# Kernel optimization log

Hardware: AMD Instinct MI355X
Metric: run time of the kernel (lower is better)

Reference implementation:

```python
import jax, jax.numpy as jnp
import numpy as np

C = 256
CQK = C // 8


def setup_inputs() -> dict:
    key = jax.random.key(0)
    ks = jax.random.split(key, 8)
    B, H, W = 4, 64, 64
    x = jax.random.normal(ks[0], (B, C, H, W), dtype=jnp.float32)
    # 1x1 conv weights are plain [out_c, in_c] matrices + bias
    sq = 1.0 / np.sqrt(C)
    Wq = jax.random.uniform(ks[1], (CQK, C), jnp.float32, -sq, sq)
    bq = jax.random.uniform(ks[2], (CQK,), jnp.float32, -sq, sq)
    Wk = jax.random.uniform(ks[3], (CQK, C), jnp.float32, -sq, sq)
    bk = jax.random.uniform(ks[4], (CQK,), jnp.float32, -sq, sq)
    Wv = jax.random.uniform(ks[5], (C, C), jnp.float32, -sq, sq)
    bv = jax.random.uniform(ks[6], (C,), jnp.float32, -sq, sq)
    gamma = jnp.zeros((1,), dtype=jnp.float32)
    return {"x": x, "Wq": Wq, "bq": bq, "Wk": Wk, "bk": bk, "Wv": Wv, "bv": bv, "gamma": gamma}


def reference(x, Wq, bq, Wk, bk, Wv, bv, gamma):
    B, Cc, H, W = x.shape
    N = H * W
    xf = x.reshape(B, Cc, N)  # [B, C, N]
    # 1x1 convs == channel GEMMs
    q = jnp.einsum('dc,bcn->bdn', Wq, xf) + bq[None, :, None]  # [B, C/8, N]
    k = jnp.einsum('dc,bcn->bdn', Wk, xf) + bk[None, :, None]  # [B, C/8, N]
    v = jnp.einsum('dc,bcn->bdn', Wv, xf) + bv[None, :, None]  # [B, C, N]
    # attention[b, i, j] = softmax_j( q_i . k_j )  (no scaling, as in source)
    attn = jax.nn.softmax(jnp.einsum('bdn,bdm->bnm', q, k), axis=-1)  # [B, N, N]
    # out = value @ attention  (note: NOT attention^T, faithful to source)
    out = jnp.einsum('bcn,bnm->bcm', v, attn)  # [B, C, N]
    out = out.reshape(B, Cc, H, W)
    return gamma[0] * out + x
```

## Files before the change

kernel.cpp:

```cpp
#include <hip/hip_runtime.h>
#include <hip/hip_bf16.h>


#define NB 4
#define CC 256
#define NN 4096
#define L2E 1.44269504088896340f

typedef short  short4v  __attribute__((ext_vector_type(4)));
typedef short  short8v  __attribute__((ext_vector_type(8)));
typedef __bf16 bf16x8   __attribute__((ext_vector_type(8)));
typedef float  f32x4    __attribute__((ext_vector_type(4)));
typedef float  f32x16   __attribute__((ext_vector_type(16)));
typedef unsigned long u64x2 __attribute__((ext_vector_type(2)));
typedef unsigned int u32;

static __device__ __forceinline__ unsigned short f2bf(float f) {
  union { __bf16 h; unsigned short u; } v; v.h = (__bf16)f; return v.u;
}
static __device__ __forceinline__ float bf2f(unsigned short u) {
  union { unsigned u; float f; } v; v.u = (u32)u << 16; return v.f;
}

union FragU { short8v s; bf16x8 b; unsigned u[4]; };

static __device__ __forceinline__ bf16x8 ld_frag(const unsigned short* p) {
  FragU u; u.s = *(const short8v*)p; return u.b;
}

static __device__ __forceinline__ f32x16 zero16() {
  f32x16 v;
#pragma unroll
  for (int i = 0; i < 16; ++i) v[i] = 0.0f;
  return v;
}

static __device__ __forceinline__ f32x16 mfma32(bf16x8 a, bf16x8 b, f32x16 c) {
  return __builtin_amdgcn_mfma_f32_32x32x16_bf16(a, b, c, 0, 0, 0);
}
static __device__ __forceinline__ f32x16 mfma8(long a, long b, f32x16 c) {
  return __builtin_amdgcn_mfma_f32_32x32x16_fp8_fp8(a, b, c, 0, 0, 0);
}

__global__ __launch_bounds__(256) void k_wcvt(
    const float* __restrict__ Wq, const float* __restrict__ Wk,
    const float* __restrict__ Wv, unsigned short* __restrict__ Wb)
{
  const int i4 = blockIdx.x * 256 + threadIdx.x;
  const int e = i4 * 4;
  const int row = e >> 8, c = e & 255;
  const float* src = (row < 32) ? (Wq + row * 256 + c)
                   : (row < 64) ? (Wk + (row - 32) * 256 + c)
                                : (Wv + (row - 64) * 256 + c);
  f32x4 v = *(const f32x4*)src;
  short4v s;
#pragma unroll
  for (int j = 0; j < 4; ++j) s[j] = (short)f2bf(v[j]);
  *(short4v*)(Wb + e) = s;
}

__global__ __launch_bounds__(256) void k_proj(
    const float* __restrict__ x, const unsigned short* __restrict__ Wb,
    const float* __restrict__ bq, const float* __restrict__ bk,
    const float* __restrict__ bv,
    unsigned short* __restrict__ Qt, unsigned short* __restrict__ Kt,
    unsigned char* __restrict__ V8)
{
  __shared__ unsigned short xs[32][268];
  const int t = threadIdx.x;
  const int b = blockIdx.y;
  const int n0 = blockIdx.x * 32;
  const int w = t >> 6, l = t & 63, h = l >> 5, col = l & 31;

  const float* xb = x + (size_t)b * CC * NN;
  {
    const int c_off = t >> 3, nl = 4 * (t & 7);
#pragma unroll
    for (int c0 = 0; c0 < CC; c0 += 32) {
      int c = c0 + c_off;
      f32x4 v4 = *(const f32x4*)(xb + (size_t)c * NN + n0 + nl);
#pragma unroll
      for (int j = 0; j < 4; ++j) xs[nl + j][c] = f2bf(v4[j]);
    }
  }
  __syncthreads();

  for (int f = w; f < 10; f += 4) {
    const float* bsrc; int rowbase; int mode; int wrow;
    if (f == 0)      { bsrc = bq; rowbase = 0;            mode = 0; wrow = 0; }
    else if (f == 1) { bsrc = bk; rowbase = 0;            mode = 1; wrow = 32; }
    else             { bsrc = bv; rowbase = (f - 2) * 32; mode = 2; wrow = 64 + rowbase; }

    f32x16 acc0 = zero16();
    const unsigned short* wr = Wb + (size_t)(wrow + col) * 256 + 8 * h;

#pragma unroll
    for (int k0 = 0; k0 < CC; k0 += 16) {
      FragU a;
      a.s = *(const short8v*)(wr + k0);
      const unsigned short* p0 = &xs[col][k0 + 8 * h];
      FragU b0;
      short4v t0a = *(const short4v*)p0, t0b = *(const short4v*)(p0 + 4);
#pragma unroll
      for (int j = 0; j < 4; ++j) { b0.s[j] = t0a[j]; b0.s[4 + j] = t0b[j]; }
      acc0 = mfma32(a.b, b0.b, acc0);
    }

    const int n = n0 + col;
#pragma unroll
    for (int q = 0; q < 4; ++q) {
      f32x4 bias4 = *(const f32x4*)(bsrc + rowbase + 8 * q + 4 * h);
      float vals[4];
#pragma unroll
      for (int i = 0; i < 4; ++i) vals[i] = acc0[4 * q + i] + bias4[i];
      if (mode == 2) {
        const size_t tb = ((((size_t)b * 128 + (n >> 5)) * 2 + ((n >> 3) & 1)) * 256) * 16
                          + ((n >> 4) & 1) * 8 + (n & 7);
        u32 w01 = __builtin_amdgcn_cvt_pk_fp8_f32(vals[0], vals[1], 0, false);
        u32 w23 = __builtin_amdgcn_cvt_pk_fp8_f32(vals[2], vals[3], 0, false);
        const int cb0 = rowbase + 8 * q + 4 * h;
        V8[tb + (size_t)(cb0 + 0) * 16] = (unsigned char)(w01 & 0xff);
        V8[tb + (size_t)(cb0 + 1) * 16] = (unsigned char)((w01 >> 8) & 0xff);
        V8[tb + (size_t)(cb0 + 2) * 16] = (unsigned char)(w23 & 0xff);
        V8[tb + (size_t)(cb0 + 3) * 16] = (unsigned char)((w23 >> 8) & 0xff);
      } else {
        unsigned short* dst = (mode == 0) ? Qt : Kt;
        const float scale = (mode == 0) ? L2E : 1.0f;
        short4v s4;
#pragma unroll
        for (int i = 0; i < 4; ++i) s4[i] = (short)f2bf(vals[i] * scale);
        *(short4v*)(dst + ((size_t)b * NN + n) * 32 + 8 * q + 4 * h) = s4;
      }
    }
  }
}

__global__ __launch_bounds__(512) void k_rowstats(
    const unsigned short* __restrict__ Qt, const unsigned short* __restrict__ Kt,
    float* __restrict__ cbias)
{
  __shared__ float ssum[8][64];
  const int t = threadIdx.x;
  const int w = t >> 6, l = t & 63, h = l >> 5, col = l & 31;
  const int b = blockIdx.y;
  const int n0 = blockIdx.x * 64;
  const unsigned short* Qb = Qt + (size_t)b * NN * 32;
  const unsigned short* Kb = Kt + (size_t)b * NN * 32;

  bf16x8 bq00 = ld_frag(Qb + (size_t)(n0 + col) * 32 + 8 * h);
  bf16x8 bq01 = ld_frag(Qb + (size_t)(n0 + col) * 32 + 16 + 8 * h);
  bf16x8 bq10 = ld_frag(Qb + (size_t)(n0 + 32 + col) * 32 + 8 * h);
  bf16x8 bq11 = ld_frag(Qb + (size_t)(n0 + 32 + col) * 32 + 16 + 8 * h);

  float acc0 = 0.0f, acc1 = 0.0f;
  const int mbase = w * (NN / 8);
#pragma unroll 2
  for (int mt = 0; mt < 16; ++mt) {
    const int m0 = mbase + mt * 32;
    bf16x8 ak0 = ld_frag(Kb + (size_t)(m0 + col) * 32 + 8 * h);
    bf16x8 ak1 = ld_frag(Kb + (size_t)(m0 + col) * 32 + 16 + 8 * h);
    f32x16 S0 = zero16(), S1 = zero16();
    S0 = mfma32(ak0, bq00, S0);
    S0 = mfma32(ak1, bq01, S0);
    S1 = mfma32(ak0, bq10, S1);
    S1 = mfma32(ak1, bq11, S1);
    float p0 = 0.0f, p1 = 0.0f, p2 = 0.0f, p3 = 0.0f;
#pragma unroll
    for (int r = 0; r < 8; ++r) {
      p0 += __builtin_amdgcn_exp2f(S0[r]);
      p1 += __builtin_amdgcn_exp2f(S0[8 + r]);
      p2 += __builtin_amdgcn_exp2f(S1[r]);
      p3 += __builtin_amdgcn_exp2f(S1[8 + r]);
    }
    acc0 += p0 + p1;
    acc1 += p2 + p3;
  }
  acc0 += __shfl_xor(acc0, 32);
  acc1 += __shfl_xor(acc1, 32);

  if (l < 32) { ssum[w][l] = acc0; ssum[w][32 + l] = acc1; }
  __syncthreads();

  if (t < 64) {
    float s = 0.0f;
#pragma unroll
    for (int wv = 0; wv < 8; ++wv) s += ssum[wv][t];
    cbias[(size_t)b * NN + n0 + t] = -__builtin_amdgcn_logf(s);
  }
}

__global__ __launch_bounds__(512) void k_emat(
    const unsigned short* __restrict__ Qt, const unsigned short* __restrict__ Kt,
    const float* __restrict__ cbias, unsigned char* __restrict__ E8)
{
  const int t = threadIdx.x;
  const int w = t >> 6, l = t & 63, h = l >> 5, col = l & 31;
  const int b = blockIdx.y;
  const int n0 = blockIdx.x * 32;
  const unsigned short* Qb = Qt + (size_t)b * NN * 32;
  const unsigned short* Kb = Kt + (size_t)b * NN * 32;

  bf16x8 aq0 = ld_frag(Qb + (size_t)(n0 + col) * 32 + 8 * h);
  bf16x8 aq1 = ld_frag(Qb + (size_t)(n0 + col) * 32 + 16 + 8 * h);

  f32x4 cb4[4];
  const float* cbi = cbias + (size_t)b * NN + n0;
#pragma unroll
  for (int q = 0; q < 4; ++q) cb4[q] = *(const f32x4*)(cbi + 8 * q + 4 * h);

  unsigned char* st = E8 + ((size_t)b * 512 + 2 * (size_t)(n0 >> 4) + h) * 32768;

#pragma unroll 2
  for (int mt = 0; mt < 16; ++mt) {
    const int m0 = w * 512 + mt * 32;
    bf16x8 bk0 = ld_frag(Kb + (size_t)(m0 + col) * 32 + 8 * h);
    bf16x8 bk1 = ld_frag(Kb + (size_t)(m0 + col) * 32 + 16 + 8 * h);
    f32x16 S = zero16();
    S = mfma32(aq0, bk0, S);
    S = mfma32(aq1, bk1, S);

    float e[16];
#pragma unroll
    for (int q = 0; q < 4; ++q)
#pragma unroll
      for (int i = 0; i < 4; ++i)
        e[4 * q + i] = __builtin_amdgcn_exp2f(S[4 * q + i] + cb4[q][i]);

    u32 wA = __builtin_amdgcn_cvt_pk_fp8_f32(e[0], e[1], 0, false);
    wA = __builtin_amdgcn_cvt_pk_fp8_f32(e[2], e[3], wA, true);
    u32 wB = __builtin_amdgcn_cvt_pk_fp8_f32(e[4], e[5], 0, false);
    wB = __builtin_amdgcn_cvt_pk_fp8_f32(e[6], e[7], wB, true);
    u32 wC = __builtin_amdgcn_cvt_pk_fp8_f32(e[8], e[9], 0, false);
    wC = __builtin_amdgcn_cvt_pk_fp8_f32(e[10], e[11], wC, true);
    u32 wD = __builtin_amdgcn_cvt_pk_fp8_f32(e[12], e[13], 0, false);
    wD = __builtin_amdgcn_cvt_pk_fp8_f32(e[14], e[15], wD, true);
    asm("v_permlane32_swap_b32 %0, %1" : "+v"(wA), "+v"(wB));
    asm("v_permlane32_swap_b32 %0, %1" : "+v"(wC), "+v"(wD));
    unsigned long ev0 = ((unsigned long)wB << 32) | wA;
    unsigned long ev1 = ((unsigned long)wD << 32) | wC;

    *(unsigned long*)(st + (size_t)(m0 + col) * 8) = ev0;
    *(unsigned long*)(st + 65536 + (size_t)(m0 + col) * 8) = ev1;
  }
}

__global__ __launch_bounds__(512) void k_pv(
    const unsigned char* __restrict__ E8, const unsigned char* __restrict__ V8,
    const float* __restrict__ x, const float* __restrict__ gamma,
    float* __restrict__ out)
{
  __shared__ unsigned short ldb[64][264];
  const int t = threadIdx.x;
  const int w = t >> 6, l = t & 63, h = l >> 5, col = l & 31;
  const int b = blockIdx.y;
  const int m0 = blockIdx.x * 64;
  const int mf = w & 1, cc = (w >> 1) * 64;

  const unsigned char* ep = E8 + ((size_t)b * 512 + h) * 32768
                            + (size_t)(m0 + mf * 32 + col) * 8;
  const unsigned char* vp = V8 + ((size_t)b * 256 + h) * 4096
                            + (size_t)(cc + col) * 16;

  f32x16 acc[2];
  acc[0] = zero16();
  acc[1] = zero16();

#pragma unroll 4
  for (int nt = 0; nt < 128; ++nt) {
    unsigned long e0 = *(const unsigned long*)(ep);
    unsigned long e1 = *(const unsigned long*)(ep + 65536);
    u64x2 vA = *(const u64x2*)(vp);
    u64x2 vB = *(const u64x2*)(vp + 512);
    acc[0] = mfma8((long)e0, (long)vA[0], acc[0]);
    acc[1] = mfma8((long)e0, (long)vB[0], acc[1]);
    acc[0] = mfma8((long)e1, (long)vA[1], acc[0]);
    acc[1] = mfma8((long)e1, (long)vB[1], acc[1]);
    ep += 131072;
    vp += 8192;
  }

#pragma unroll
  for (int cf = 0; cf < 2; ++cf)
#pragma unroll
    for (int r = 0; r < 16; ++r) {
      int mloc = mf * 32 + (r & 3) + 8 * (r >> 2) + 4 * h;
      ldb[mloc][cc + 32 * cf + col] = f2bf(acc[cf][r]);
    }
  __syncthreads();

  const float g = gamma[0];
  const int ci = t >> 4;
  const int m4 = (t & 15) * 4;
#pragma unroll
  for (int rnd = 0; rnd < 8; ++rnd) {
    const int c = 32 * rnd + ci;
    const size_t idx = ((size_t)b * CC + c) * NN + m0 + m4;
    f32x4 xv = *(const f32x4*)(x + idx);
    f32x4 o;
#pragma unroll
    for (int k = 0; k < 4; ++k) o[k] = g * bf2f(ldb[m4 + k][c]) + xv[k];
    *(f32x4*)(out + idx) = o;
  }
}

extern "C" void kernel_launch(void* const* d_in, const int* in_sizes, int n_in,
                              void* d_out, int out_size, void* d_ws, size_t ws_size,
                              hipStream_t stream) {
  const float* x     = (const float*)d_in[0];
  const float* Wq    = (const float*)d_in[1];
  const float* bq    = (const float*)d_in[2];
  const float* Wk    = (const float*)d_in[3];
  const float* bk    = (const float*)d_in[4];
  const float* Wv    = (const float*)d_in[5];
  const float* bv    = (const float*)d_in[6];
  const float* gamma = (const float*)d_in[7];
  float* out = (float*)d_out;

  char* ws = (char*)d_ws;
  unsigned short* Qt = (unsigned short*)(ws);
  unsigned short* Kt = (unsigned short*)(ws + (1u << 20));
  unsigned char*  V8 = (unsigned char*)(ws + (2u << 20));
  unsigned short* Wb = (unsigned short*)(ws + (6u << 20));
  float* cbias = (float*)(ws + (6u << 20) + (1u << 18));
  unsigned char* E8  = (unsigned char*)(ws + (7u << 20));

  k_wcvt<<<dim3(80), 256, 0, stream>>>(Wq, Wk, Wv, Wb);
  k_proj<<<dim3(NN / 32, NB), 256, 0, stream>>>(x, Wb, bq, bk, bv, Qt, Kt, V8);
  k_rowstats<<<dim3(NN / 64, NB), 512, 0, stream>>>(Qt, Kt, cbias);
  k_emat<<<dim3(NN / 32, NB), 512, 0, stream>>>(Qt, Kt, cbias, E8);
  k_pv<<<dim3(NN / 64, NB), 512, 0, stream>>>(E8, V8, x, gamma, out);
}
```

Before: 100.0 us.

## Halve k_pv tile per block and software-pipeline E/V loads

Result: no change. 100.7 us (+0.7%).

```diff
diff --git a/kernel.cpp b/kernel.cpp
--- a/kernel.cpp
+++ b/kernel.cpp
@@ -244,20 +244,20 @@
   }
 }
 
-__global__ __launch_bounds__(512) void k_pv(
+__global__ __launch_bounds__(256) void k_pv(
     const unsigned char* __restrict__ E8, const unsigned char* __restrict__ V8,
     const float* __restrict__ x, const float* __restrict__ gamma,
     float* __restrict__ out)
 {
-  __shared__ unsigned short ldb[64][264];
+  __shared__ unsigned short ldb[32][264];
   const int t = threadIdx.x;
   const int w = t >> 6, l = t & 63, h = l >> 5, col = l & 31;
   const int b = blockIdx.y;
-  const int m0 = blockIdx.x * 64;
-  const int mf = w & 1, cc = (w >> 1) * 64;
+  const int m0 = blockIdx.x * 32;
+  const int cc = w * 64;
 
   const unsigned char* ep = E8 + ((size_t)b * 512 + h) * 32768
-                            + (size_t)(m0 + mf * 32 + col) * 8;
+                            + (size_t)(m0 + col) * 8;
   const unsigned char* vp = V8 + ((size_t)b * 256 + h) * 4096
                             + (size_t)(cc + col) * 16;
 
@@ -265,32 +265,42 @@
   acc[0] = zero16();
   acc[1] = zero16();
 
+  unsigned long e0c = *(const unsigned long*)(ep);
+  unsigned long e1c = *(const unsigned long*)(ep + 65536);
+  u64x2 vAc = *(const u64x2*)(vp);
+  u64x2 vBc = *(const u64x2*)(vp + 512);
+  ep += 131072; vp += 8192;
+
 #pragma unroll 4
-  for (int nt = 0; nt < 128; ++nt) {
-    unsigned long e0 = *(const unsigned long*)(ep);
-    unsigned long e1 = *(const unsigned long*)(ep + 65536);
-    u64x2 vA = *(const u64x2*)(vp);
-    u64x2 vB = *(const u64x2*)(vp + 512);
-    acc[0] = mfma8((long)e0, (long)vA[0], acc[0]);
-    acc[1] = mfma8((long)e0, (long)vB[0], acc[1]);
-    acc[0] = mfma8((long)e1, (long)vA[1], acc[0]);
-    acc[1] = mfma8((long)e1, (long)vB[1], acc[1]);
-    ep += 131072;
-    vp += 8192;
-  }
+  for (int nt = 0; nt < 127; ++nt) {
+    unsigned long e0n = *(const unsigned long*)(ep);
+    unsigned long e1n = *(const unsigned long*)(ep + 65536);
+    u64x2 vAn = *(const u64x2*)(vp);
+    u64x2 vBn = *(const u64x2*)(vp + 512);
+    ep += 131072; vp += 8192;
+    acc[0] = mfma8((long)e0c, (long)vAc[0], acc[0]);
+    acc[1] = mfma8((long)e0c, (long)vBc[0], acc[1]);
+    acc[0] = mfma8((long)e1c, (long)vAc[1], acc[0]);
+    acc[1] = mfma8((long)e1c, (long)vBc[1], acc[1]);
+    e0c = e0n; e1c = e1n; vAc = vAn; vBc = vBn;
+  }
+  acc[0] = mfma8((long)e0c, (long)vAc[0], acc[0]);
+  acc[1] = mfma8((long)e0c, (long)vBc[0], acc[1]);
+  acc[0] = mfma8((long)e1c, (long)vAc[1], acc[0]);
+  acc[1] = mfma8((long)e1c, (long)vBc[1], acc[1]);
 
 #pragma unroll
   for (int cf = 0; cf < 2; ++cf)
 #pragma unroll
     for (int r = 0; r < 16; ++r) {
-      int mloc = mf * 32 + (r & 3) + 8 * (r >> 2) + 4 * h;
+      int mloc = (r & 3) + 8 * (r >> 2) + 4 * h;
       ldb[mloc][cc + 32 * cf + col] = f2bf(acc[cf][r]);
     }
   __syncthreads();
 
   const float g = gamma[0];
-  const int ci = t >> 4;
-  const int m4 = (t & 15) * 4;
+  const int ci = t >> 3;
+  const int m4 = (t & 7) * 4;
 #pragma unroll
   for (int rnd = 0; rnd < 8; ++rnd) {
     const int c = 32 * rnd + ci;
@@ -328,5 +338,5 @@
   k_proj<<<dim3(NN / 32, NB), 256, 0, stream>>>(x, Wb, bq, bk, bv, Qt, Kt, V8);
   k_rowstats<<<dim3(NN / 64, NB), 512, 0, stream>>>(Qt, Kt, cbias);
   k_emat<<<dim3(NN / 32, NB), 512, 0, stream>>>(Qt, Kt, cbias, E8);
-  k_pv<<<dim3(NN / 64, NB), 512, 0, stream>>>(E8, V8, x, gamma, out);
-}
+  k_pv<<<dim3(NN / 32, NB), 256, 0, stream>>>(E8, V8, x, gamma, out);
+}
```
